# Optimization experiments

Hardware: AMD Instinct MI355X
Metric: run time of the kernel (lower is better)

Reference implementation:

```python
import jax, jax.numpy as jnp
import numpy as np
import math

D_MODEL = 128
N_HEAD = 8
D_K = D_MODEL // N_HEAD
NEG_INF = -1e30


def setup_inputs() -> dict:
    key = jax.random.key(0)
    ks = jax.random.split(key, 8)
    B, N, D = 4, 2048, D_MODEL
    s = 1.0 / math.sqrt(D)
    x = jax.random.normal(ks[0], (B, D, N), dtype=jnp.float32)
    mask = jnp.ones((B, N), dtype=jnp.float32)
    Wq = jax.random.normal(ks[1], (D, D), dtype=jnp.float32) * s
    Wk = jax.random.normal(ks[2], (D, D), dtype=jnp.float32) * s
    Wv = jax.random.normal(ks[3], (D, D), dtype=jnp.float32) * s
    Wfc = jax.random.normal(ks[4], (D, D), dtype=jnp.float32) * s
    z = jnp.zeros((D,), dtype=jnp.float32)
    return {"x": x, "mask": mask, "Wq": Wq, "bq": z, "Wk": Wk, "bk": z,
            "Wv": Wv, "bv": z, "Wfc": Wfc, "bfc": z}


def reference(x, mask, Wq, bq, Wk, bk, Wv, bv, Wfc, bfc):
    # x: [B, D, N], mask: [B, N]
    B, D, N = x.shape
    xt = jnp.swapaxes(x, 1, 2)  # [B, N, D]
    q = (xt @ Wq.T + bq).reshape(B, N, N_HEAD, D_K)
    k = (xt @ Wk.T + bk).reshape(B, N, N_HEAD, D_K)
    v = (xt @ Wv.T + bv).reshape(B, N, N_HEAD, D_K)
    # scores: [B, H, Nq, Nk]; NOTE: original scales by sqrt(d_model), not sqrt(d_k)
    scores = jnp.einsum('bnhd,bmhd->bhnm', q, k) / jnp.sqrt(jnp.float32(D))
    # multiplicative mask_logits over the key dimension
    m = mask[:, None, None, :]  # [B, 1, 1, Nk]
    scores = scores * m + (1.0 - m) * NEG_INF
    atten = jax.nn.softmax(scores, axis=-1)  # dropout is identity (p=0 / eval)
    out = jnp.einsum('bhnm,bmhd->bnhd', atten, v).reshape(B, N, D)
    out = out @ Wfc.T + bfc
    return jnp.swapaxes(out, 1, 2)  # [B, D, N]
```

## Files before the change

kernel.cpp:

```cpp
#include <hip/hip_runtime.h>
#include <stdint.h>

#define BSZ  4
#define NSEQ 2048
#define DM   128
#define NH   8
#define DK   16
#define LOG2E 1.4426950408889634f
#define SCALE_QL 0.1275156338341935f
#define W_SCALE 3.814697265625e-6f

typedef __bf16          bf16x8v __attribute__((ext_vector_type(8)));
typedef float           f32x4   __attribute__((ext_vector_type(4)));
typedef float           f32x16  __attribute__((ext_vector_type(16)));
typedef unsigned short  u16x8   __attribute__((ext_vector_type(8)));
typedef unsigned short  u16x4   __attribute__((ext_vector_type(4)));
typedef unsigned int    u32x2   __attribute__((ext_vector_type(2)));
typedef unsigned int    u32x4   __attribute__((ext_vector_type(4)));

__device__ __forceinline__ unsigned short f2bf(float f) {
    unsigned u = __float_as_uint(f);
    u = (u + 0x7fffu + ((u >> 16) & 1u)) >> 16;
    return (unsigned short)u;
}

__device__ __forceinline__ unsigned int pack2bf(float a, float b) {
#if __has_builtin(__builtin_amdgcn_cvt_pk_bf16_f32)
    typedef __bf16 bf16x2 __attribute__((ext_vector_type(2)));
    bf16x2 v = __builtin_amdgcn_cvt_pk_bf16_f32(a, b);
    return __builtin_bit_cast(unsigned int, v);
#else
    return (unsigned)f2bf(a) | ((unsigned)f2bf(b) << 16);
#endif
}

__device__ __forceinline__ float exp2_(float x) {
#if __has_builtin(__builtin_amdgcn_exp2f)
    return __builtin_amdgcn_exp2f(x);
#else
    return exp2f(x);
#endif
}

__device__ __forceinline__ u16x8 cvt8(const float* p, float sc) {
    const f32x4 a = *reinterpret_cast<const f32x4*>(p);
    const f32x4 b = *reinterpret_cast<const f32x4*>(p + 4);
    u32x4 u = {pack2bf(a[0] * sc, a[1] * sc), pack2bf(a[2] * sc, a[3] * sc),
               pack2bf(b[0] * sc, b[1] * sc), pack2bf(b[2] * sc, b[3] * sc)};
    return __builtin_bit_cast(u16x8, u);
}

__device__ __forceinline__ f32x4 mfma16(u16x8 a, u16x8 b, f32x4 c) {
    return __builtin_amdgcn_mfma_f32_16x16x32_bf16(
        __builtin_bit_cast(bf16x8v, a), __builtin_bit_cast(bf16x8v, b), c, 0, 0, 0);
}
__device__ __forceinline__ f32x16 mfma32(u16x8 a, u16x8 b, f32x16 c) {
    return __builtin_amdgcn_mfma_f32_32x32x16_bf16(
        __builtin_bit_cast(bf16x8v, a), __builtin_bit_cast(bf16x8v, b), c, 0, 0, 0);
}

__global__ __launch_bounds__(768) void k_qkv(
    const float* __restrict__ x,
    const float* __restrict__ Wq, const float* __restrict__ bq,
    const float* __restrict__ Wk, const float* __restrict__ bk,
    const float* __restrict__ Wv, const float* __restrict__ bv,
    const float* __restrict__ Wfc, const float* __restrict__ mask,
    unsigned short* __restrict__ Q, unsigned short* __restrict__ Kb,
    unsigned short* __restrict__ Vt,
    unsigned short* __restrict__ WfcB, unsigned short* __restrict__ wb)
{
    __shared__ __align__(16) float xs[DM * 36];
    const int tid = threadIdx.x;

    const int gt = blockIdx.x * 768 + tid;
    if (gt < DM * DM) {
        WfcB[gt] = f2bf(Wfc[gt]);
    } else if (gt < DM * DM + BSZ * NSEQ) {
        const int i = gt - DM * DM;
        wb[i] = f2bf(mask[i] * W_SCALE);
    }

    const int b  = blockIdx.x >> 6;
    const int n0 = (blockIdx.x & 63) << 5;

#pragma unroll
    for (int i = tid; i < 1024; i += 768) {
        const int d = i >> 3, c4 = (i & 7) << 2;
        *reinterpret_cast<f32x4*>(&xs[d * 36 + c4]) =
            *reinterpret_cast<const f32x4*>(x + (size_t)(b * DM + d) * NSEQ + n0 + c4);
    }
    __syncthreads();

    const int lane = tid & 63;
    const int wv   = tid >> 6;
    const int mat  = wv >> 2;
    const int nt   = (wv >> 1) & 1;
    const int th   = wv & 1;
    const int c    = lane & 15;
    const int quad = lane >> 4;
    const int col  = n0 + nt * 16 + c;

    u16x8 xf[4];
#pragma unroll
    for (int kk = 0; kk < 4; ++kk) {
        float f[8];
#pragma unroll
        for (int j = 0; j < 8; ++j)
            f[j] = xs[(kk * 32 + quad * 8 + j) * 36 + nt * 16 + c];
        u32x4 u = {pack2bf(f[0], f[1]), pack2bf(f[2], f[3]),
                   pack2bf(f[4], f[5]), pack2bf(f[6], f[7])};
        xf[kk] = __builtin_bit_cast(u16x8, u);
    }

    const float* W    = (mat == 0) ? Wq : (mat == 1) ? Wk : Wv;
    const float* bias = (mat == 0) ? bq : (mat == 1) ? bk : bv;
    const float  sc   = (mat == 0) ? SCALE_QL : 1.0f;
    const float  vw   = (mat == 2) ? mask[b * NSEQ + col] * W_SCALE : 0.f;

#pragma unroll
    for (int tt = 0; tt < 4; ++tt) {
        const int t = th * 4 + tt;
        f32x4 acc = {0.f, 0.f, 0.f, 0.f};
#pragma unroll
        for (int kk = 0; kk < 4; ++kk)
            acc = mfma16(cvt8(W + (t * 16 + c) * DM + kk * 32 + quad * 8, sc),
                         xf[kk], acc);
        if (mat == 2) {
#pragma unroll
            for (int r = 0; r < 4; ++r)
                Vt[((b * NH + t) * DK + quad * 4 + r) * NSEQ + col] =
                    f2bf((acc[r] + bias[t * 16 + quad * 4 + r]) * vw);
        } else {
            u16x4 pk;
#pragma unroll
            for (int r = 0; r < 4; ++r)
                pk[r] = f2bf(acc[r] + bias[t * 16 + quad * 4 + r] * sc);
            *reinterpret_cast<u16x4*>(
                (mat == 0 ? Q : Kb) + ((size_t)(b * NH + t) * NSEQ + col) * DK +
                quad * 4) = pk;
        }
    }
}

__global__ __launch_bounds__(256, 4) void k_attn(
    const unsigned short* __restrict__ Q,
    const unsigned short* __restrict__ Kb,
    const unsigned short* __restrict__ Vt,
    const unsigned short* __restrict__ wb,
    unsigned short* __restrict__ AO)
{
    __shared__ __align__(16) char smem[17408];
    const int tid  = threadIdx.x;
    const int lane = tid & 63;
    const int w    = tid >> 6;
    const int q32  = lane & 31;
    const int c    = lane & 15;
    const int quad = lane >> 4;
    const int hi   = lane >> 5;

    const int bid = ((int)blockIdx.x & 7) * 256 + ((int)blockIdx.x >> 3);
    const int b  = bid >> 9;
    const int h  = (bid >> 6) & 7;
    const int n0 = (bid & 63) << 5;
    const int bh = b * NH + h;

    const u16x8 uq = *reinterpret_cast<const u16x8*>(
        Q + ((size_t)bh * NSEQ + n0 + q32) * DK + 8 * hi);

    const unsigned short* Kp = Kb + (size_t)bh * NSEQ * DK + 8 * hi;
    const unsigned short* Vp = Vt + ((size_t)bh * DK + c) * NSEQ + 8 * quad;
    const unsigned short* wp = wb + b * NSEQ + 8 * quad;

    char* pb = smem + w * 4352;
    const int wroff  = q32 * 136 + 8 * hi;
    const int rd0off = c * 136 + 16 * quad;
    const int rd1off = (c + 16) * 136 + 16 * quad;

    f32x4 o0 = {0.f, 0.f, 0.f, 0.f}, o1 = {0.f, 0.f, 0.f, 0.f};
    f32x4 l0 = {0.f, 0.f, 0.f, 0.f}, l1 = {0.f, 0.f, 0.f, 0.f};
    const f32x16 z16 = {};
    const int kvb = w * (NSEQ / 4);

    u16x8 nk0 = *reinterpret_cast<const u16x8*>(Kp + (size_t)(kvb + q32) * DK);
    u16x8 nk1 = *reinterpret_cast<const u16x8*>(Kp + (size_t)(kvb + 32 + q32) * DK);

    auto stage = [&](const int it) {
        const int kv0 = kvb + it * 64;
        __builtin_amdgcn_s_setprio(1);
        f32x16 S0 = mfma32(nk0, uq, z16);
        f32x16 S1 = mfma32(nk1, uq, z16);
        __builtin_amdgcn_s_setprio(0);
        if (it < 7) {
            nk0 = *reinterpret_cast<const u16x8*>(Kp + (size_t)(kv0 + 64 + q32) * DK);
            nk1 = *reinterpret_cast<const u16x8*>(Kp + (size_t)(kv0 + 96 + q32) * DK);
        }
#pragma unroll
        for (int i = 0; i < 16; ++i) {
            S0[i] = exp2_(S0[i]);
            S1[i] = exp2_(S1[i]);
        }
        char* wrow = pb + wroff;
#pragma unroll
        for (int g = 0; g < 4; ++g) {
            u32x2 d0 = {pack2bf(S0[4 * g], S0[4 * g + 1]),
                        pack2bf(S0[4 * g + 2], S0[4 * g + 3])};
            u32x2 d1 = {pack2bf(S1[4 * g], S1[4 * g + 1]),
                        pack2bf(S1[4 * g + 2], S1[4 * g + 3])};
            *reinterpret_cast<u32x2*>(wrow + 16 * g) = d0;
            *reinterpret_cast<u32x2*>(wrow + 64 + 16 * g) = d1;
        }
    };

    stage(0);

#pragma unroll 2
    for (int it = 0; it < 8; ++it) {
        const int kv0 = kvb + it * 64;

        const char* ra = pb + rd0off;
        const char* rb = pb + rd1off;
        const u16x8 up0a = *reinterpret_cast<const u16x8*>(ra);
        const u16x8 up1a = *reinterpret_cast<const u16x8*>(rb);
        const u16x8 up0b = *reinterpret_cast<const u16x8*>(ra + 64);
        const u16x8 up1b = *reinterpret_cast<const u16x8*>(rb + 64);
        const u16x8 uv0 = *reinterpret_cast<const u16x8*>(Vp + kv0);
        const u16x8 uv1 = *reinterpret_cast<const u16x8*>(Vp + kv0 + 32);

        if (it < 7) stage(it + 1);

        const u16x8 uw0 = *reinterpret_cast<const u16x8*>(wp + kv0);
        const u16x8 uw1 = *reinterpret_cast<const u16x8*>(wp + kv0 + 32);

        __builtin_amdgcn_s_setprio(1);
        o0 = mfma16(uv0, up0a, o0);
        o1 = mfma16(uv0, up1a, o1);
        l0 = mfma16(uw0, up0a, l0);
        l1 = mfma16(uw0, up1a, l1);
        o0 = mfma16(uv1, up0b, o0);
        o1 = mfma16(uv1, up1b, o1);
        l0 = mfma16(uw1, up0b, l0);
        l1 = mfma16(uw1, up1b, l1);
        __builtin_amdgcn_s_setprio(0);
    }

    __syncthreads();
    float* Lsm = reinterpret_cast<float*>(smem);
    float* Osm = reinterpret_cast<float*>(smem + 512);
    Lsm[w * 32 + c]      = l0[0];
    Lsm[w * 32 + 16 + c] = l1[0];
    *reinterpret_cast<f32x4*>(Osm + w * 640 + c * 20 + 4 * quad)        = o0;
    *reinterpret_cast<f32x4*>(Osm + w * 640 + (c + 16) * 20 + 4 * quad) = o1;
    __syncthreads();

    const int q   = tid >> 3;
    const int dk2 = (tid & 7) * 2;
    const float l = Lsm[q] + Lsm[32 + q] + Lsm[64 + q] + Lsm[96 + q];
    const float* Oq = Osm + q * 20 + dk2;
    const float v0 = Oq[0] + Oq[640] + Oq[1280] + Oq[1920];
    const float v1 = Oq[1] + Oq[641] + Oq[1281] + Oq[1921];
    const float inv = 1.0f / l;
    *reinterpret_cast<unsigned int*>(
        AO + ((size_t)(b * NSEQ) + n0 + q) * DM + h * DK + dk2) =
        pack2bf(v0 * inv, v1 * inv);
}

__global__ __launch_bounds__(256) void k_fc(
    const unsigned short* __restrict__ AO,
    const unsigned short* __restrict__ WfcB, const float* __restrict__ bfc,
    float* __restrict__ out)
{
    const int lane = threadIdx.x & 63;
    const int w    = threadIdx.x >> 6;
    const int c    = lane & 15;
    const int quad = lane >> 4;
    const int b    = blockIdx.x >> 8;
    const int n0   = ((blockIdx.x >> 1) & 127) << 4;
    const int t    = (blockIdx.x & 1) * 4 + w;

    u16x8 af[4];
#pragma unroll
    for (int kk = 0; kk < 4; ++kk)
        af[kk] = *reinterpret_cast<const u16x8*>(
            AO + ((size_t)(b * NSEQ) + n0 + c) * DM + kk * 32 + quad * 8);

    f32x4 acc = {0.f, 0.f, 0.f, 0.f};
#pragma unroll
    for (int kk = 0; kk < 4; ++kk)
        acc = mfma16(*reinterpret_cast<const u16x8*>(
                         WfcB + (t * 16 + c) * DM + kk * 32 + quad * 8),
                     af[kk], acc);
#pragma unroll
    for (int r = 0; r < 4; ++r)
        out[(size_t)(b * DM + t * 16 + quad * 4 + r) * NSEQ + n0 + c] =
            acc[r] + bfc[t * 16 + quad * 4 + r];
}

extern "C" void kernel_launch(void* const* d_in, const int* in_sizes, int n_in,
                              void* d_out, int out_size, void* d_ws, size_t ws_size,
                              hipStream_t stream)
{
    const float* x    = (const float*)d_in[0];
    const float* mask = (const float*)d_in[1];
    const float* Wq   = (const float*)d_in[2];
    const float* bq   = (const float*)d_in[3];
    const float* Wk   = (const float*)d_in[4];
    const float* bk   = (const float*)d_in[5];
    const float* Wv   = (const float*)d_in[6];
    const float* bv   = (const float*)d_in[7];
    const float* Wfc  = (const float*)d_in[8];
    const float* bfc  = (const float*)d_in[9];
    float* out = (float*)d_out;

    const size_t QKV_ELEMS = (size_t)BSZ * NH * NSEQ * DK;
    unsigned short* Q    = (unsigned short*)d_ws;
    unsigned short* Kb   = Q + QKV_ELEMS;
    unsigned short* Vt   = Kb + QKV_ELEMS;
    unsigned short* AO   = Vt + QKV_ELEMS;
    unsigned short* WfcB = AO + QKV_ELEMS;
    unsigned short* wb   = WfcB + DM * DM;

    k_qkv<<<256, 768, 0, stream>>>(x, Wq, bq, Wk, bk, Wv, bv, Wfc, mask,
                                   Q, Kb, Vt, WfcB, wb);
    k_attn<<<2048, 256, 0, stream>>>(Q, Kb, Vt, wb, AO);
    k_fc<<<1024, 256, 0, stream>>>(AO, WfcB, bfc, out);
}
```

Measured before the change: 129.6 us.

## Drop software pipelining of score stage to cut registers and raise occupancy

Removes the one-iteration-ahead pipelining of the QK^T/exp/LDS-write stage. Each iteration now computes its scores in two sequential halves before reading P back from LDS, and the loop is no longer unrolled. Launch bounds rise from 4 to 6 waves per SIMD. The aim is lower register pressure and more resident waves to hide latency, at the cost of intra-wave overlap between score computation and the PV MFMAs. Each wave reads back only its own LDS rows, and the per-wave buffer layout looks unchanged.

```diff
diff --git a/kernel.cpp b/kernel.cpp
--- a/kernel.cpp
+++ b/kernel.cpp
@@ -142,7 +142,7 @@
     }
 }
 
-__global__ __launch_bounds__(256, 4) void k_attn(
+__global__ __launch_bounds__(256, 6) void k_attn(
     const unsigned short* __restrict__ Q,
     const unsigned short* __restrict__ Kb,
     const unsigned short* __restrict__ Vt,
@@ -172,9 +172,9 @@
     const unsigned short* wp = wb + b * NSEQ + 8 * quad;
 
     char* pb = smem + w * 4352;
-    const int wroff  = q32 * 136 + 8 * hi;
-    const int rd0off = c * 136 + 16 * quad;
-    const int rd1off = (c + 16) * 136 + 16 * quad;
+    char* wrow = pb + q32 * 136 + 8 * hi;
+    const char* rrow0 = pb + c * 136 + 16 * quad;
+    const char* rrow1 = pb + (c + 16) * 136 + 16 * quad;
 
     f32x4 o0 = {0.f, 0.f, 0.f, 0.f}, o1 = {0.f, 0.f, 0.f, 0.f};
     f32x4 l0 = {0.f, 0.f, 0.f, 0.f}, l1 = {0.f, 0.f, 0.f, 0.f};
@@ -184,50 +184,51 @@
     u16x8 nk0 = *reinterpret_cast<const u16x8*>(Kp + (size_t)(kvb + q32) * DK);
     u16x8 nk1 = *reinterpret_cast<const u16x8*>(Kp + (size_t)(kvb + 32 + q32) * DK);
 
-    auto stage = [&](const int it) {
-        const int kv0 = kvb + it * 64;
-        __builtin_amdgcn_s_setprio(1);
-        f32x16 S0 = mfma32(nk0, uq, z16);
-        f32x16 S1 = mfma32(nk1, uq, z16);
-        __builtin_amdgcn_s_setprio(0);
-        if (it < 7) {
-            nk0 = *reinterpret_cast<const u16x8*>(Kp + (size_t)(kv0 + 64 + q32) * DK);
-            nk1 = *reinterpret_cast<const u16x8*>(Kp + (size_t)(kv0 + 96 + q32) * DK);
-        }
-#pragma unroll
-        for (int i = 0; i < 16; ++i) {
-            S0[i] = exp2_(S0[i]);
-            S1[i] = exp2_(S1[i]);
-        }
-        char* wrow = pb + wroff;
-#pragma unroll
-        for (int g = 0; g < 4; ++g) {
-            u32x2 d0 = {pack2bf(S0[4 * g], S0[4 * g + 1]),
-                        pack2bf(S0[4 * g + 2], S0[4 * g + 3])};
-            u32x2 d1 = {pack2bf(S1[4 * g], S1[4 * g + 1]),
-                        pack2bf(S1[4 * g + 2], S1[4 * g + 3])};
-            *reinterpret_cast<u32x2*>(wrow + 16 * g) = d0;
-            *reinterpret_cast<u32x2*>(wrow + 64 + 16 * g) = d1;
-        }
-    };
-
-    stage(0);
-
-#pragma unroll 2
+#pragma unroll 1
     for (int it = 0; it < 8; ++it) {
         const int kv0 = kvb + it * 64;
 
-        const char* ra = pb + rd0off;
-        const char* rb = pb + rd1off;
-        const u16x8 up0a = *reinterpret_cast<const u16x8*>(ra);
-        const u16x8 up1a = *reinterpret_cast<const u16x8*>(rb);
-        const u16x8 up0b = *reinterpret_cast<const u16x8*>(ra + 64);
-        const u16x8 up1b = *reinterpret_cast<const u16x8*>(rb + 64);
         const u16x8 uv0 = *reinterpret_cast<const u16x8*>(Vp + kv0);
         const u16x8 uv1 = *reinterpret_cast<const u16x8*>(Vp + kv0 + 32);
 
-        if (it < 7) stage(it + 1);
-
+        {
+            __builtin_amdgcn_s_setprio(1);
+            f32x16 S0 = mfma32(nk0, uq, z16);
+            __builtin_amdgcn_s_setprio(0);
+            if (it < 7)
+                nk0 = *reinterpret_cast<const u16x8*>(
+                    Kp + (size_t)(kv0 + 64 + q32) * DK);
+#pragma unroll
+            for (int i = 0; i < 16; ++i) S0[i] = exp2_(S0[i]);
+#pragma unroll
+            for (int g = 0; g < 4; ++g) {
+                u32x2 d = {pack2bf(S0[4 * g], S0[4 * g + 1]),
+                           pack2bf(S0[4 * g + 2], S0[4 * g + 3])};
+                *reinterpret_cast<u32x2*>(wrow + 16 * g) = d;
+            }
+        }
+
+        {
+            __builtin_amdgcn_s_setprio(1);
+            f32x16 S1 = mfma32(nk1, uq, z16);
+            __builtin_amdgcn_s_setprio(0);
+            if (it < 7)
+                nk1 = *reinterpret_cast<const u16x8*>(
+                    Kp + (size_t)(kv0 + 96 + q32) * DK);
+#pragma unroll
+            for (int i = 0; i < 16; ++i) S1[i] = exp2_(S1[i]);
+#pragma unroll
+            for (int g = 0; g < 4; ++g) {
+                u32x2 d = {pack2bf(S1[4 * g], S1[4 * g + 1]),
+                           pack2bf(S1[4 * g + 2], S1[4 * g + 3])};
+                *reinterpret_cast<u32x2*>(wrow + 64 + 16 * g) = d;
+            }
+        }
+
+        const u16x8 up0a = *reinterpret_cast<const u16x8*>(rrow0);
+        const u16x8 up1a = *reinterpret_cast<const u16x8*>(rrow1);
+        const u16x8 up0b = *reinterpret_cast<const u16x8*>(rrow0 + 64);
+        const u16x8 up1b = *reinterpret_cast<const u16x8*>(rrow1 + 64);
         const u16x8 uw0 = *reinterpret_cast<const u16x8*>(wp + kv0);
         const u16x8 uw1 = *reinterpret_cast<const u16x8*>(wp + kv0 + 32);
 
```

New measurement: 130.1 us. Within noise of the previous version (+0.4%).
